# Performance work log

Hardware: AMD Instinct MI355X
Metric: run time of the kernel (lower is better)

Reference implementation:

```python
import jax, jax.numpy as jnp
import numpy as np
import math

B, C, K, H, W_SP = 16, 512, 64, 64, 64
STAGE_NUM = 2
THETA = 45


def _l2norm(x, axis):
    return x / (1e-6 + jnp.linalg.norm(x, axis=axis, keepdims=True))


def setup_inputs() -> dict:
    key = jax.random.key(0)
    k1, k2, k3, k4 = jax.random.split(key, 4)
    x = jax.random.normal(k1, (B, C, H, W_SP), dtype=jnp.float32)
    # conv1: 1x1 conv with bias, He init n = 1*1*C
    W1 = jax.random.normal(k2, (C, C), dtype=jnp.float32) * math.sqrt(2.0 / C)
    b1 = jnp.zeros((C,), dtype=jnp.float32)
    # conv2: 1x1 conv no bias + BN(gamma=1, beta=0)
    W2 = jax.random.normal(k3, (C, C), dtype=jnp.float32) * math.sqrt(2.0 / C)
    gamma = jnp.ones((C,), dtype=jnp.float32)
    beta = jnp.zeros((C,), dtype=jnp.float32)
    # mu buffer: normal(0, sqrt(2/k)), l2-normalized over channel dim
    mu0 = jax.random.normal(k4, (1, C, K), dtype=jnp.float32) * math.sqrt(2.0 / K)
    mu0 = _l2norm(mu0, axis=1)
    return {"x": x, "W1": W1, "b1": b1, "W2": W2, "gamma": gamma, "beta": beta, "mu0": mu0}


def reference(x, W1, b1, W2, gamma, beta, mu0):
    idn = x
    # conv1 (1x1)
    xc = jnp.einsum('bchw,oc->bohw', x, W1) + b1[None, :, None, None]
    b, c, h, w = xc.shape
    xf = xc.reshape(b, c, h * w)  # [b, c, n]
    mu = jnp.broadcast_to(mu0, (b, c, K))
    alpha0 = math.sin(math.radians(THETA)) ** 2
    beta0 = math.cos(math.radians(THETA)) ** 2
    v = K - 1
    # EM loop runs under torch.no_grad in the original -> stop_gradient
    xs = jax.lax.stop_gradient(xf)
    z = None
    for _ in range(STAGE_NUM):
        z = jnp.einsum('bcn,bck->bnk', xs, mu)  # [b, n, k]
        # V-E step: softmax / power-law blend
        z = alpha0 * jax.nn.softmax(z, axis=2) \
            + beta0 * (v + 1) / (v + 2.0 * jnp.linalg.norm(z, axis=2, keepdims=True))
        z_ = z / (1e-6 + z.sum(axis=1, keepdims=True))
        # V-M step
        mu = _l2norm(jnp.einsum('bcn,bnk->bck', xs, z_), axis=1)
    mu = jax.lax.stop_gradient(mu)
    z = jax.lax.stop_gradient(z)
    # reconstruction
    xr = jnp.einsum('bck,bnk->bcn', mu, z).reshape(b, c, h, w)
    xr = jax.nn.relu(xr)
    # conv2 (1x1, no bias) + BN (training-mode batch stats, eps=1e-5)
    y = jnp.einsum('bchw,oc->bohw', xr, W2)
    mean = y.mean(axis=(0, 2, 3))
    var = y.var(axis=(0, 2, 3))
    y = gamma[None, :, None, None] * (y - mean[None, :, None, None]) \
        * jax.lax.rsqrt(var + 1e-5)[None, :, None, None] + beta[None, :, None, None]
    out = jax.nn.relu(y + idn)
    return (out, mu, jnp.float32(THETA))
```

## Files before the change

### kernel.cpp

```cpp
#include <hip/hip_runtime.h>
#include <hip/hip_bf16.h>

#define B_ 16
#define C_ 512
#define K_ 64
#define N_ 4096
#define LDA 40

typedef unsigned short ushort_t;
typedef __attribute__((ext_vector_type(8))) short s16x8;
typedef __attribute__((ext_vector_type(4))) short s16x4;
typedef __attribute__((ext_vector_type(4))) float f32x4;

__device__ inline ushort_t f2bf(float f) {
    unsigned int u = __builtin_bit_cast(unsigned int, f);
    u = (u + 0x7FFFu + ((u >> 16) & 1u)) >> 16;
    return (ushort_t)u;
}
__device__ inline ushort_t f2bf_fast(float f) {
    unsigned int u = __builtin_bit_cast(unsigned int, f);
    return (ushort_t)((u + 0x8000u) >> 16);
}
__device__ inline float bf2f(ushort_t h) {
    unsigned int u = ((unsigned int)h) << 16;
    return __builtin_bit_cast(float, u);
}

template<int R>
__device__ inline void stage_tile(ushort_t* lds, const ushort_t* g, int gstride) {
    const int t = threadIdx.x;
    #pragma unroll
    for (int l = 0; l < R / 64; ++l) {
        int ch = t + l * 256;
        int row = ch >> 2, seg = ch & 3;
        s16x8 v = *(const s16x8*)(g + (size_t)row * gstride + seg * 8);
        *(s16x8*)(lds + row * LDA + seg * 8) = v;
    }
}

__global__ __launch_bounds__(256)
void cvtW_kernel(const float* __restrict__ W1, const float* __restrict__ W2,
                 ushort_t* __restrict__ W1b, ushort_t* __restrict__ W2b)
{
    int idx = blockIdx.x * 256 + threadIdx.x;
    const float* s; ushort_t* d; int off;
    if (idx < 32768) { s = W1; d = W1b; off = idx * 8; }
    else             { s = W2; d = W2b; off = (idx - 32768) * 8; }
    float4 a = *(const float4*)(s + off);
    float4 b = *(const float4*)(s + off + 4);
    s16x8 v;
    v[0] = (short)f2bf(a.x); v[1] = (short)f2bf(a.y);
    v[2] = (short)f2bf(a.z); v[3] = (short)f2bf(a.w);
    v[4] = (short)f2bf(b.x); v[5] = (short)f2bf(b.y);
    v[6] = (short)f2bf(b.z); v[7] = (short)f2bf(b.w);
    *(s16x8*)(d + off) = v;
}

__global__ __launch_bounds__(256)
void initmu_kernel(const float* __restrict__ mu0, ushort_t* __restrict__ mu_t)
{
    int idx = blockIdx.x * 256 + threadIdx.x;
    float v = mu0[idx];
    mu_t[(idx & 63) * C_ + (idx >> 6)] = f2bf(v);
}

__global__ __launch_bounds__(256)
void conv1_mfma(const ushort_t* __restrict__ W1b, const float* __restrict__ x,
                const float* __restrict__ b1, ushort_t* __restrict__ xf,
                ushort_t* __restrict__ xft)
{
    __shared__ ushort_t As[128 * LDA];
    __shared__ ushort_t Bs[128 * LDA];
    const int n0 = blockIdx.x * 128;
    const int o0 = blockIdx.y * 128;
    const int b  = blockIdx.z;
    const int t  = threadIdx.x;
    const int wid = t >> 6, lane = t & 63;
    const int wm = wid >> 1, wn = wid & 1;
    const int l15 = lane & 15, q = lane >> 4;

    const ushort_t* gA = W1b + (size_t)o0 * C_;
    const float*    xB = x + (size_t)b * C_ * N_ + n0;
    const int cg = t >> 5, ng = t & 31;

    f32x4 acc[4][4] = {};

    for (int c0 = 0; c0 < C_; c0 += 32) {
        __syncthreads();
        stage_tile<128>(As, gA + c0, C_);
        {
            const float* src = xB + (size_t)(c0 + cg * 4) * N_ + ng * 4;
            float4 f0 = *(const float4*)(src);
            float4 f1 = *(const float4*)(src + N_);
            float4 f2 = *(const float4*)(src + 2 * N_);
            float4 f3 = *(const float4*)(src + 3 * N_);
            ushort_t* dst = Bs + (ng * 4) * LDA + cg * 4;
            s16x4 v;
            v[0] = (short)f2bf_fast(f0.x); v[1] = (short)f2bf_fast(f1.x);
            v[2] = (short)f2bf_fast(f2.x); v[3] = (short)f2bf_fast(f3.x);
            *(s16x4*)(dst) = v;
            v[0] = (short)f2bf_fast(f0.y); v[1] = (short)f2bf_fast(f1.y);
            v[2] = (short)f2bf_fast(f2.y); v[3] = (short)f2bf_fast(f3.y);
            *(s16x4*)(dst + LDA) = v;
            v[0] = (short)f2bf_fast(f0.z); v[1] = (short)f2bf_fast(f1.z);
            v[2] = (short)f2bf_fast(f2.z); v[3] = (short)f2bf_fast(f3.z);
            *(s16x4*)(dst + 2 * LDA) = v;
            v[0] = (short)f2bf_fast(f0.w); v[1] = (short)f2bf_fast(f1.w);
            v[2] = (short)f2bf_fast(f2.w); v[3] = (short)f2bf_fast(f3.w);
            *(s16x4*)(dst + 3 * LDA) = v;
        }
        __syncthreads();
        s16x8 af[4], bf[4];
        #pragma unroll
        for (int m = 0; m < 4; ++m)
            af[m] = *(const s16x8*)&As[(wm * 64 + m * 16 + l15) * LDA + q * 8];
        #pragma unroll
        for (int n = 0; n < 4; ++n)
            bf[n] = *(const s16x8*)&Bs[(wn * 64 + n * 16 + l15) * LDA + q * 8];
        #pragma unroll
        for (int m = 0; m < 4; ++m)
            #pragma unroll
            for (int n = 0; n < 4; ++n)
                acc[m][n] = __builtin_amdgcn_mfma_f32_16x16x32_bf16(af[m], bf[n], acc[m][n], 0, 0, 0);
    }

    ushort_t* xfB  = xf  + (size_t)b * C_ * N_;
    ushort_t* xftB = xft + (size_t)b * N_ * C_;
    #pragma unroll
    for (int m = 0; m < 4; ++m) {
        int obase = o0 + wm * 64 + m * 16 + 4 * q;
        float bv[4];
        #pragma unroll
        for (int r = 0; r < 4; ++r) bv[r] = b1[obase + r];
        #pragma unroll
        for (int n = 0; n < 4; ++n) {
            int nn = n0 + wn * 64 + n * 16 + l15;
            s16x4 pk;
            #pragma unroll
            for (int r = 0; r < 4; ++r) {
                ushort_t h = f2bf(acc[m][n][r] + bv[r]);
                pk[r] = (short)h;
                xfB[(size_t)(obase + r) * N_ + nn] = h;
            }
            *(s16x4*)&xftB[(size_t)nn * C_ + obase] = pk;
        }
    }
}

__global__ __launch_bounds__(256)
void zfused_mfma(const ushort_t* __restrict__ mu_t, const ushort_t* __restrict__ xft,
                 ushort_t* __restrict__ zst, ushort_t* __restrict__ zs,
                 float* __restrict__ cs, int mustride)
{
    __shared__ char pool[64 * 133 * 4 + 64 * 132 * 2 + 128 * 2 * 4];
    float*    zt  = (float*)pool;
    ushort_t* zb  = (ushort_t*)(pool + 64 * 133 * 4);
    float*    csb = (float*)(pool + 64 * 133 * 4 + 64 * 132 * 2);
    ushort_t* As  = (ushort_t*)pool;
    ushort_t* Bs  = (ushort_t*)(pool + 64 * LDA * 2);

    const int n0 = blockIdx.x * 128;
    const int b  = blockIdx.y;
    const int t  = threadIdx.x;
    const int wid = t >> 6, lane = t & 63;
    const int wm = wid >> 1, wn = wid & 1;
    const int l15 = lane & 15, q = lane >> 4;

    const ushort_t* gA = mu_t + (size_t)b * mustride;
    const ushort_t* gB = xft + (size_t)b * N_ * C_ + (size_t)n0 * C_;

    f32x4 acc[2][4] = {};

    for (int c0 = 0; c0 < C_; c0 += 32) {
        __syncthreads();
        stage_tile<64>(As, gA + c0, C_);
        stage_tile<128>(Bs, gB + c0, C_);
        __syncthreads();
        s16x8 af[2], bf[4];
        #pragma unroll
        for (int m = 0; m < 2; ++m)
            af[m] = *(const s16x8*)&As[(wm * 32 + m * 16 + l15) * LDA + q * 8];
        #pragma unroll
        for (int n = 0; n < 4; ++n)
            bf[n] = *(const s16x8*)&Bs[(wn * 64 + n * 16 + l15) * LDA + q * 8];
        #pragma unroll
        for (int m = 0; m < 2; ++m)
            #pragma unroll
            for (int n = 0; n < 4; ++n)
                acc[m][n] = __builtin_amdgcn_mfma_f32_16x16x32_bf16(af[m], bf[n], acc[m][n], 0, 0, 0);
    }

    __syncthreads();
    #pragma unroll
    for (int m = 0; m < 2; ++m) {
        int kbase = wm * 32 + m * 16 + 4 * q;
        #pragma unroll
        for (int n = 0; n < 4; ++n) {
            int nl = wn * 64 + n * 16 + l15;
            #pragma unroll
            for (int r = 0; r < 4; ++r)
                zt[(kbase + r) * 133 + nl] = acc[m][n][r];
        }
    }
    __syncthreads();
    if (t < 128) {
        const float* col = zt + t;
        float mx = -1e30f, sq = 0.f;
        #pragma unroll
        for (int k = 0; k < K_; ++k) {
            float v = col[k * 133];
            mx = fmaxf(mx, v);
            sq += v * v;
        }
        float se = 0.f;
        #pragma unroll
        for (int k = 0; k < K_; ++k) {
            float e = __expf(col[k * 133] - mx);
            se += e;
            zb[k * 132 + t] = f2bf(e);
        }
        csb[t * 2]     = 0.5f / se;
        csb[t * 2 + 1] = 0.5f * 64.f / (63.f + 2.f * sqrtf(sq));
    }
    __syncthreads();
    ushort_t* zstB = zst + (size_t)b * K_ * N_;
    #pragma unroll
    for (int i = 0; i < 4; ++i) {
        int ch = t + 256 * i;
        int k = ch >> 4, seg = ch & 15;
        s16x8 e8 = *(const s16x8*)&zb[k * 132 + seg * 8];
        s16x8 o8;
        float sum = 0.f;
        #pragma unroll
        for (int j = 0; j < 8; ++j) {
            int nl = seg * 8 + j;
            float v = fmaf(bf2f((ushort_t)e8[j]), csb[nl * 2], csb[nl * 2 + 1]);
            sum += v;
            o8[j] = (short)f2bf(v);
        }
        *(s16x8*)&zstB[(size_t)k * N_ + n0 + seg * 8] = o8;
        #pragma unroll
        for (int off = 1; off < 16; off <<= 1) sum += __shfl_xor(sum, off);
        if ((t & 15) == 0) atomicAdd(&cs[b * K_ + k], sum);
    }
    ushort_t* zsB = zs + (size_t)b * N_ * K_;
    #pragma unroll
    for (int i = 0; i < 4; ++i) {
        int ch = t + 256 * i;
        int nl = ch >> 3, kseg = ch & 7;
        float sc = csb[nl * 2], bl = csb[nl * 2 + 1];
        s16x8 o8;
        #pragma unroll
        for (int j = 0; j < 8; ++j) {
            int j2 = (j + nl) & 7;
            float v = fmaf(bf2f(zb[(kseg * 8 + j2) * 132 + nl]), sc, bl);
            o8[j2] = (short)f2bf(v);
        }
        *(s16x8*)&zsB[(size_t)(n0 + nl) * K_ + kseg * 8] = o8;
    }
}

__global__ __launch_bounds__(256)
void mugemm_mfma(const ushort_t* __restrict__ zst, const ushort_t* __restrict__ xf,
                 const float* __restrict__ cs, float* __restrict__ macc)
{
    __shared__ ushort_t As[64 * LDA];
    __shared__ ushort_t Bs[128 * LDA];
    const int ns = blockIdx.x * 512;
    const int c0 = blockIdx.y * 128;
    const int b  = blockIdx.z;
    const int t  = threadIdx.x;
    const int wid = t >> 6, lane = t & 63;
    const int wm = wid >> 1, wn = wid & 1;
    const int l15 = lane & 15, q = lane >> 4;

    const ushort_t* gA = zst + (size_t)b * K_ * N_ + ns;
    const ushort_t* gB = xf + (size_t)b * C_ * N_ + (size_t)c0 * N_ + ns;

    f32x4 acc[2][4] = {};

    for (int nn0 = 0; nn0 < 512; nn0 += 32) {
        __syncthreads();
        stage_tile<64>(As, gA + nn0, N_);
        stage_tile<128>(Bs, gB + nn0, N_);
        __syncthreads();
        s16x8 af[2], bf[4];
        #pragma unroll
        for (int m = 0; m < 2; ++m)
            af[m] = *(const s16x8*)&As[(wm * 32 + m * 16 + l15) * LDA + q * 8];
        #pragma unroll
        for (int n = 0; n < 4; ++n)
            bf[n] = *(const s16x8*)&Bs[(wn * 64 + n * 16 + l15) * LDA + q * 8];
        #pragma unroll
        for (int m = 0; m < 2; ++m)
            #pragma unroll
            for (int n = 0; n < 4; ++n)
                acc[m][n] = __builtin_amdgcn_mfma_f32_16x16x32_bf16(af[m], bf[n], acc[m][n], 0, 0, 0);
    }

    float* mB = macc + (size_t)b * K_ * C_;
    #pragma unroll
    for (int m = 0; m < 2; ++m) {
        int kbase = wm * 32 + m * 16 + 4 * q;
        float ic[4];
        #pragma unroll
        for (int r = 0; r < 4; ++r) ic[r] = 1.f / (1e-6f + cs[b * K_ + kbase + r]);
        #pragma unroll
        for (int n = 0; n < 4; ++n) {
            int cc = c0 + wn * 64 + n * 16 + l15;
            #pragma unroll
            for (int r = 0; r < 4; ++r)
                atomicAdd(&mB[(size_t)(kbase + r) * C_ + cc], acc[m][n][r] * ic[r]);
        }
    }
}

__global__ __launch_bounds__(256)
void l2norm_t(const float* __restrict__ macc, ushort_t* __restrict__ mu_t,
              ushort_t* __restrict__ mu_b, float* __restrict__ mu_out,
              float* __restrict__ theta_out)
{
    int wid  = blockIdx.x * 4 + (threadIdx.x >> 6);
    int lane = threadIdx.x & 63;
    int b = wid >> 6, k = wid & 63;
    const float* src = macc + (size_t)b * K_ * C_ + (size_t)k * C_;
    float v[8], s = 0.f;
    #pragma unroll
    for (int i = 0; i < 8; ++i) { v[i] = src[lane + i * 64]; s += v[i] * v[i]; }
    #pragma unroll
    for (int off = 32; off > 0; off >>= 1) s += __shfl_xor(s, off);
    float inv = 1.f / (1e-6f + sqrtf(s));
    ushort_t* mt = mu_t + (size_t)b * K_ * C_ + (size_t)k * C_;
    ushort_t* mb = mu_b + (size_t)b * C_ * K_ + k;
    float*    mo = mu_out + (size_t)b * C_ * K_ + k;
    #pragma unroll
    for (int i = 0; i < 8; ++i) {
        int c = lane + i * 64;
        float val = v[i] * inv;
        mt[c] = f2bf(val);
        mb[(size_t)c * K_] = f2bf(val);
        mo[(size_t)c * K_] = val;
    }
    if (wid == 0 && lane == 0) *theta_out = 45.0f;
}

__global__ __launch_bounds__(256)
void recon_mfma(const ushort_t* __restrict__ mu_b, const ushort_t* __restrict__ zs,
                ushort_t* __restrict__ xrt)
{
    __shared__ ushort_t As[128 * LDA];
    __shared__ ushort_t Bs[128 * LDA];
    const int n0 = blockIdx.x * 128;
    const int c0 = blockIdx.y * 128;
    const int b  = blockIdx.z;
    const int t  = threadIdx.x;
    const int wid = t >> 6, lane = t & 63;
    const int wm = wid >> 1, wn = wid & 1;
    const int l15 = lane & 15, q = lane >> 4;

    const ushort_t* gA = mu_b + (size_t)b * C_ * K_ + (size_t)c0 * K_;
    const ushort_t* gB = zs + (size_t)b * N_ * K_ + (size_t)n0 * K_;

    f32x4 acc[4][4] = {};

    for (int k0 = 0; k0 < K_; k0 += 32) {
        __syncthreads();
        stage_tile<128>(As, gA + k0, K_);
        stage_tile<128>(Bs, gB + k0, K_);
        __syncthreads();
        s16x8 af[4], bf[4];
        #pragma unroll
        for (int m = 0; m < 4; ++m)
            af[m] = *(const s16x8*)&As[(wm * 64 + m * 16 + l15) * LDA + q * 8];
        #pragma unroll
        for (int n = 0; n < 4; ++n)
            bf[n] = *(const s16x8*)&Bs[(wn * 64 + n * 16 + l15) * LDA + q * 8];
        #pragma unroll
        for (int m = 0; m < 4; ++m)
            #pragma unroll
            for (int n = 0; n < 4; ++n)
                acc[m][n] = __builtin_amdgcn_mfma_f32_16x16x32_bf16(af[m], bf[n], acc[m][n], 0, 0, 0);
    }

    ushort_t* xB = xrt + (size_t)b * N_ * C_;
    #pragma unroll
    for (int m = 0; m < 4; ++m) {
        int cbase = c0 + wm * 64 + m * 16 + 4 * q;
        #pragma unroll
        for (int n = 0; n < 4; ++n) {
            int nn = n0 + wn * 64 + n * 16 + l15;
            s16x4 pk;
            #pragma unroll
            for (int r = 0; r < 4; ++r)
                pk[r] = (short)f2bf(fmaxf(acc[m][n][r], 0.f));
            *(s16x4*)&xB[(size_t)nn * C_ + cbase] = pk;
        }
    }
}

__global__ __launch_bounds__(256)
void conv2_mfma(const ushort_t* __restrict__ W2b, const ushort_t* __restrict__ xrt,
                float* __restrict__ y, float* __restrict__ ysum, float* __restrict__ ysq)
{
    __shared__ ushort_t As[128 * LDA];
    __shared__ ushort_t Bs[128 * LDA];
    __shared__ float sums[128][2];
    const int n0 = blockIdx.x * 128;
    const int o0 = blockIdx.y * 128;
    const int b  = blockIdx.z;
    const int t  = threadIdx.x;
    const int wid = t >> 6, lane = t & 63;
    const int wm = wid >> 1, wn = wid & 1;
    const int l15 = lane & 15, q = lane >> 4;

    const ushort_t* gA = W2b + (size_t)o0 * C_;
    const ushort_t* gB = xrt + (size_t)b * N_ * C_ + (size_t)n0 * C_;

    f32x4 acc[4][4] = {};

    for (int c0 = 0; c0 < C_; c0 += 32) {
        __syncthreads();
        stage_tile<128>(As, gA + c0, C_);
        stage_tile<128>(Bs, gB + c0, C_);
        __syncthreads();
        s16x8 af[4], bf[4];
        #pragma unroll
        for (int m = 0; m < 4; ++m)
            af[m] = *(const s16x8*)&As[(wm * 64 + m * 16 + l15) * LDA + q * 8];
        #pragma unroll
        for (int n = 0; n < 4; ++n)
            bf[n] = *(const s16x8*)&Bs[(wn * 64 + n * 16 + l15) * LDA + q * 8];
        #pragma unroll
        for (int m = 0; m < 4; ++m)
            #pragma unroll
            for (int n = 0; n < 4; ++n)
                acc[m][n] = __builtin_amdgcn_mfma_f32_16x16x32_bf16(af[m], bf[n], acc[m][n], 0, 0, 0);
    }

    float* yB = y + (size_t)b * C_ * N_;
    float ps[4][4], pq[4][4];
    #pragma unroll
    for (int m = 0; m < 4; ++m) {
        int obase = o0 + wm * 64 + m * 16 + 4 * q;
        #pragma unroll
        for (int r = 0; r < 4; ++r) { ps[m][r] = 0.f; pq[m][r] = 0.f; }
        #pragma unroll
        for (int n = 0; n < 4; ++n) {
            int nn = n0 + wn * 64 + n * 16 + l15;
            #pragma unroll
            for (int r = 0; r < 4; ++r) {
                float v = acc[m][n][r];
                yB[(size_t)(obase + r) * N_ + nn] = v;
                ps[m][r] += v;
                pq[m][r] = fmaf(v, v, pq[m][r]);
            }
        }
    }
    #pragma unroll
    for (int m = 0; m < 4; ++m)
        #pragma unroll
        for (int r = 0; r < 4; ++r)
            #pragma unroll
            for (int off = 1; off < 16; off <<= 1) {
                ps[m][r] += __shfl_xor(ps[m][r], off);
                pq[m][r] += __shfl_xor(pq[m][r], off);
            }
    __syncthreads();
    if (l15 == 0 && wn == 0) {
        #pragma unroll
        for (int m = 0; m < 4; ++m)
            #pragma unroll
            for (int r = 0; r < 4; ++r) {
                int ol = wm * 64 + m * 16 + 4 * q + r;
                sums[ol][0] = ps[m][r];
                sums[ol][1] = pq[m][r];
            }
    }
    __syncthreads();
    if (l15 == 0 && wn == 1) {
        #pragma unroll
        for (int m = 0; m < 4; ++m)
            #pragma unroll
            for (int r = 0; r < 4; ++r) {
                int ol = wm * 64 + m * 16 + 4 * q + r;
                sums[ol][0] += ps[m][r];
                sums[ol][1] += pq[m][r];
            }
    }
    __syncthreads();
    if (t < 128) {
        atomicAdd(&ysum[o0 + t], sums[t][0]);
        atomicAdd(&ysq[o0 + t],  sums[t][1]);
    }
}

__global__ __launch_bounds__(256)
void bnout_kernel(float* __restrict__ y, const float* __restrict__ x,
                  const float* __restrict__ gamma, const float* __restrict__ beta,
                  const float* __restrict__ ysum, const float* __restrict__ ysq)
{
    size_t i = (size_t)blockIdx.x * 256 + threadIdx.x;
    float4 vy = ((float4*)y)[i];
    float4 vx = ((const float4*)x)[i];
    int o = (int)((i >> 10) & (C_ - 1));
    const float inv_n = 1.f / (float)(B_ * N_);
    float mean = ysum[o] * inv_n;
    float var  = ysq[o] * inv_n - mean * mean;
    float istd = rsqrtf(var + 1e-5f);
    float sc = gamma[o] * istd;
    float sh = beta[o] - sc * mean;
    float4 r;
    r.x = fmaxf(fmaf(vy.x, sc, sh) + vx.x, 0.f);
    r.y = fmaxf(fmaf(vy.y, sc, sh) + vx.y, 0.f);
    r.z = fmaxf(fmaf(vy.z, sc, sh) + vx.z, 0.f);
    r.w = fmaxf(fmaf(vy.w, sc, sh) + vx.w, 0.f);
    ((float4*)y)[i] = r;
}

extern "C" void kernel_launch(void* const* d_in, const int* in_sizes, int n_in,
                              void* d_out, int out_size, void* d_ws, size_t ws_size,
                              hipStream_t stream)
{
    const float* x     = (const float*)d_in[0];
    const float* W1    = (const float*)d_in[1];
    const float* b1    = (const float*)d_in[2];
    const float* W2    = (const float*)d_in[3];
    const float* gamma = (const float*)d_in[4];
    const float* beta  = (const float*)d_in[5];
    const float* mu0   = (const float*)d_in[6];

    char* w = (char*)d_ws;
    ushort_t* xf   = (ushort_t*)w;  w += (size_t)B_ * C_ * N_ * 2;
    ushort_t* xft  = (ushort_t*)w;  w += (size_t)B_ * N_ * C_ * 2;
    ushort_t* W1b  = (ushort_t*)w;  w += (size_t)C_ * C_ * 2;
    ushort_t* W2b  = (ushort_t*)w;  w += (size_t)C_ * C_ * 2;
    ushort_t* mu_t = (ushort_t*)w;  w += (size_t)B_ * K_ * C_ * 2;
    ushort_t* mu_b = (ushort_t*)w;  w += (size_t)B_ * C_ * K_ * 2;
    float* cs      = (float*)w;     w += (size_t)B_ * K_ * 4;
    float* macc    = (float*)w;     w += (size_t)B_ * K_ * C_ * 4;
    float* ysum    = (float*)w;     w += C_ * 4;
    float* ysq     = (float*)w;     w += C_ * 4;

    ushort_t* xrt = xf;

    float* y         = (float*)d_out;
    float* mu_out    = (float*)d_out + (size_t)B_ * C_ * N_;
    float* theta_out = mu_out + (size_t)B_ * C_ * K_;
    ushort_t* zst = (ushort_t*)(y + (size_t)8  * 1024 * 1024);
    ushort_t* zs  = (ushort_t*)(y + (size_t)16 * 1024 * 1024);

    cvtW_kernel<<<256, 256, 0, stream>>>(W1, W2, W1b, W2b);
    initmu_kernel<<<128, 256, 0, stream>>>(mu0, mu_t);
    hipMemsetAsync(ysum, 0, 2 * C_ * 4, stream);

    conv1_mfma<<<dim3(32, 4, 16), 256, 0, stream>>>(W1b, x, b1, xf, xft);

    for (int s = 0; s < 2; ++s) {
        hipMemsetAsync(cs, 0, (size_t)B_ * K_ * 4 + (size_t)B_ * K_ * C_ * 4, stream);
        zfused_mfma<<<dim3(32, 16), 256, 0, stream>>>(mu_t, xft, zst, zs, cs,
                                                      s == 0 ? 0 : K_ * C_);
        mugemm_mfma<<<dim3(8, 4, 16), 256, 0, stream>>>(zst, xf, cs, macc);
        l2norm_t<<<256, 256, 0, stream>>>(macc, mu_t, mu_b, mu_out, theta_out);
    }

    recon_mfma<<<dim3(32, 4, 16), 256, 0, stream>>>(mu_b, zs, xrt);
    conv2_mfma<<<dim3(32, 4, 16), 256, 0, stream>>>(W2b, xrt, y, ysum, ysq);
    bnout_kernel<<<dim3(B_ * C_ * N_ / 4 / 256), 256, 0, stream>>>(y, x, gamma, beta, ysum, ysq);
}
```

Baseline: 573.4 us.

## Stage conv GEMM tiles via direct global-to-LDS loads with XOR-swizzled layouts

Adds a separate kernel that converts x to transposed bf16 with an XOR-swizzled channel layout. conv1 and conv2 now stage tiles with global_load_lds 16-byte transfers into unpadded LDS instead of register round trips. W1/W2 conversion and recon output are written in the same swizzled order so LDS fragment reads avoid bank conflicts without padding. This adds an extra pass over x and reuses the output buffer as scratch, in exchange for cheaper GEMM staging.

```diff
diff --git a/kernel.cpp b/kernel.cpp
--- a/kernel.cpp
+++ b/kernel.cpp
@@ -24,6 +24,12 @@
 __device__ inline float bf2f(ushort_t h) {
     unsigned int u = ((unsigned int)h) << 16;
     return __builtin_bit_cast(float, u);
+}
+
+__device__ inline void gload16(const ushort_t* g, ushort_t* l) {
+    __builtin_amdgcn_global_load_lds(
+        (const __attribute__((address_space(1))) void*)g,
+        (__attribute__((address_space(3))) void*)l, 16, 0, 0);
 }
 
 template<int R>
@@ -53,7 +59,9 @@
     v[2] = (short)f2bf(a.z); v[3] = (short)f2bf(a.w);
     v[4] = (short)f2bf(b.x); v[5] = (short)f2bf(b.y);
     v[6] = (short)f2bf(b.z); v[7] = (short)f2bf(b.w);
-    *(s16x8*)(d + off) = v;
+    int o = off >> 9, c = off & 511;
+    int dst = o * C_ + (c & ~31) + 8 * (((c >> 3) & 3) ^ ((o >> 1) & 3));
+    *(s16x8*)(d + dst) = v;
 }
 
 __global__ __launch_bounds__(256)
@@ -65,12 +73,52 @@
 }
 
 __global__ __launch_bounds__(256)
-void conv1_mfma(const ushort_t* __restrict__ W1b, const float* __restrict__ x,
+void xcvt_kernel(const float* __restrict__ x, ushort_t* __restrict__ xbt)
+{
+    __shared__ __align__(16) ushort_t lds[64 * 72];
+    const int n0 = blockIdx.x * 64;
+    const int c0 = blockIdx.y * 64;
+    const int b  = blockIdx.z;
+    const int t  = threadIdx.x;
+    const int cq = t >> 4, nq = t & 15;
+    const float* src = x + ((size_t)b * C_ + c0 + cq * 4) * N_ + n0 + nq * 4;
+    float4 f0 = *(const float4*)(src);
+    float4 f1 = *(const float4*)(src + N_);
+    float4 f2 = *(const float4*)(src + 2 * N_);
+    float4 f3 = *(const float4*)(src + 3 * N_);
+    ushort_t* ld = lds + (nq * 4) * 72 + cq * 4;
+    s16x4 v;
+    v[0] = (short)f2bf_fast(f0.x); v[1] = (short)f2bf_fast(f1.x);
+    v[2] = (short)f2bf_fast(f2.x); v[3] = (short)f2bf_fast(f3.x);
+    *(s16x4*)(ld) = v;
+    v[0] = (short)f2bf_fast(f0.y); v[1] = (short)f2bf_fast(f1.y);
+    v[2] = (short)f2bf_fast(f2.y); v[3] = (short)f2bf_fast(f3.y);
+    *(s16x4*)(ld + 72) = v;
+    v[0] = (short)f2bf_fast(f0.z); v[1] = (short)f2bf_fast(f1.z);
+    v[2] = (short)f2bf_fast(f2.z); v[3] = (short)f2bf_fast(f3.z);
+    *(s16x4*)(ld + 144) = v;
+    v[0] = (short)f2bf_fast(f0.w); v[1] = (short)f2bf_fast(f1.w);
+    v[2] = (short)f2bf_fast(f2.w); v[3] = (short)f2bf_fast(f3.w);
+    *(s16x4*)(ld + 216) = v;
+    __syncthreads();
+    ushort_t* dst = xbt + ((size_t)b * N_ + n0) * C_ + c0;
+    #pragma unroll
+    for (int i = 0; i < 2; ++i) {
+        int ch = t + 256 * i;
+        int row = ch >> 3, seg = ch & 7;
+        s16x8 w = *(const s16x8*)&lds[row * 72 + seg * 8];
+        int cc = (seg >> 2) * 32 + 8 * ((seg & 3) ^ ((row >> 1) & 3));
+        *(s16x8*)(dst + (size_t)row * C_ + cc) = w;
+    }
+}
+
+__global__ __launch_bounds__(256)
+void conv1_mfma(const ushort_t* __restrict__ W1b, const ushort_t* __restrict__ xbt,
                 const float* __restrict__ b1, ushort_t* __restrict__ xf,
                 ushort_t* __restrict__ xft)
 {
-    __shared__ ushort_t As[128 * LDA];
-    __shared__ ushort_t Bs[128 * LDA];
+    __shared__ __align__(16) ushort_t As[128 * 32];
+    __shared__ __align__(16) ushort_t Bs[128 * 32];
     const int n0 = blockIdx.x * 128;
     const int o0 = blockIdx.y * 128;
     const int b  = blockIdx.z;
@@ -78,45 +126,33 @@
     const int wid = t >> 6, lane = t & 63;
     const int wm = wid >> 1, wn = wid & 1;
     const int l15 = lane & 15, q = lane >> 4;
+    const int gsw = (q ^ ((l15 >> 1) & 3)) * 8;
 
     const ushort_t* gA = W1b + (size_t)o0 * C_;
-    const float*    xB = x + (size_t)b * C_ * N_ + n0;
-    const int cg = t >> 5, ng = t & 31;
+    const ushort_t* gB = xbt + ((size_t)b * N_ + n0) * C_;
+    const size_t choff  = (size_t)(t >> 2) * C_ + (t & 3) * 8;
+    const size_t choff2 = choff + (size_t)64 * C_;
+
+    int aoff[4], boff[4];
+    #pragma unroll
+    for (int m = 0; m < 4; ++m) aoff[m] = (wm * 64 + m * 16 + l15) * 32 + gsw;
+    #pragma unroll
+    for (int n = 0; n < 4; ++n) boff[n] = (wn * 64 + n * 16 + l15) * 32 + gsw;
 
     f32x4 acc[4][4] = {};
 
     for (int c0 = 0; c0 < C_; c0 += 32) {
         __syncthreads();
-        stage_tile<128>(As, gA + c0, C_);
-        {
-            const float* src = xB + (size_t)(c0 + cg * 4) * N_ + ng * 4;
-            float4 f0 = *(const float4*)(src);
-            float4 f1 = *(const float4*)(src + N_);
-            float4 f2 = *(const float4*)(src + 2 * N_);
-            float4 f3 = *(const float4*)(src + 3 * N_);
-            ushort_t* dst = Bs + (ng * 4) * LDA + cg * 4;
-            s16x4 v;
-            v[0] = (short)f2bf_fast(f0.x); v[1] = (short)f2bf_fast(f1.x);
-            v[2] = (short)f2bf_fast(f2.x); v[3] = (short)f2bf_fast(f3.x);
-            *(s16x4*)(dst) = v;
-            v[0] = (short)f2bf_fast(f0.y); v[1] = (short)f2bf_fast(f1.y);
-            v[2] = (short)f2bf_fast(f2.y); v[3] = (short)f2bf_fast(f3.y);
-            *(s16x4*)(dst + LDA) = v;
-            v[0] = (short)f2bf_fast(f0.z); v[1] = (short)f2bf_fast(f1.z);
-            v[2] = (short)f2bf_fast(f2.z); v[3] = (short)f2bf_fast(f3.z);
-            *(s16x4*)(dst + 2 * LDA) = v;
-            v[0] = (short)f2bf_fast(f0.w); v[1] = (short)f2bf_fast(f1.w);
-            v[2] = (short)f2bf_fast(f2.w); v[3] = (short)f2bf_fast(f3.w);
-            *(s16x4*)(dst + 3 * LDA) = v;
-        }
+        gload16(gA + choff  + c0, &As[t * 8]);
+        gload16(gA + choff2 + c0, &As[t * 8 + 2048]);
+        gload16(gB + choff  + c0, &Bs[t * 8]);
+        gload16(gB + choff2 + c0, &Bs[t * 8 + 2048]);
         __syncthreads();
         s16x8 af[4], bf[4];
         #pragma unroll
-        for (int m = 0; m < 4; ++m)
-            af[m] = *(const s16x8*)&As[(wm * 64 + m * 16 + l15) * LDA + q * 8];
-        #pragma unroll
-        for (int n = 0; n < 4; ++n)
-            bf[n] = *(const s16x8*)&Bs[(wn * 64 + n * 16 + l15) * LDA + q * 8];
+        for (int m = 0; m < 4; ++m) af[m] = *(const s16x8*)&As[aoff[m]];
+        #pragma unroll
+        for (int n = 0; n < 4; ++n) bf[n] = *(const s16x8*)&Bs[boff[n]];
         #pragma unroll
         for (int m = 0; m < 4; ++m)
             #pragma unroll
@@ -152,7 +188,7 @@
                  ushort_t* __restrict__ zst, ushort_t* __restrict__ zs,
                  float* __restrict__ cs, int mustride)
 {
-    __shared__ char pool[64 * 133 * 4 + 64 * 132 * 2 + 128 * 2 * 4];
+    __shared__ __align__(16) char pool[64 * 133 * 4 + 64 * 132 * 2 + 128 * 2 * 4];
     float*    zt  = (float*)pool;
     ushort_t* zb  = (ushort_t*)(pool + 64 * 133 * 4);
     float*    csb = (float*)(pool + 64 * 133 * 4 + 64 * 132 * 2);
@@ -264,8 +300,8 @@
 void mugemm_mfma(const ushort_t* __restrict__ zst, const ushort_t* __restrict__ xf,
                  const float* __restrict__ cs, float* __restrict__ macc)
 {
-    __shared__ ushort_t As[64 * LDA];
-    __shared__ ushort_t Bs[128 * LDA];
+    __shared__ __align__(16) ushort_t As[64 * LDA];
+    __shared__ __align__(16) ushort_t Bs[128 * LDA];
     const int ns = blockIdx.x * 512;
     const int c0 = blockIdx.y * 128;
     const int b  = blockIdx.z;
@@ -348,8 +384,8 @@
 void recon_mfma(const ushort_t* __restrict__ mu_b, const ushort_t* __restrict__ zs,
                 ushort_t* __restrict__ xrt)
 {
-    __shared__ ushort_t As[128 * LDA];
-    __shared__ ushort_t Bs[128 * LDA];
+    __shared__ __align__(16) ushort_t As[128 * LDA];
+    __shared__ __align__(16) ushort_t Bs[128 * LDA];
     const int n0 = blockIdx.x * 128;
     const int c0 = blockIdx.y * 128;
     const int b  = blockIdx.z;
@@ -383,9 +419,11 @@
     }
 
     ushort_t* xB = xrt + (size_t)b * N_ * C_;
+    const int swn = (l15 >> 1) & 3;
     #pragma unroll
     for (int m = 0; m < 4; ++m) {
         int cbase = c0 + wm * 64 + m * 16 + 4 * q;
+        int cswz  = (cbase & ~31) + 8 * (((cbase >> 3) & 3) ^ swn) + (cbase & 7);
         #pragma unroll
         for (int n = 0; n < 4; ++n) {
             int nn = n0 + wn * 64 + n * 16 + l15;
@@ -393,7 +431,7 @@
             #pragma unroll
             for (int r = 0; r < 4; ++r)
                 pk[r] = (short)f2bf(fmaxf(acc[m][n][r], 0.f));
-            *(s16x4*)&xB[(size_t)nn * C_ + cbase] = pk;
+            *(s16x4*)&xB[(size_t)nn * C_ + cswz] = pk;
         }
     }
 }
@@ -402,8 +440,8 @@
 void conv2_mfma(const ushort_t* __restrict__ W2b, const ushort_t* __restrict__ xrt,
                 float* __restrict__ y, float* __restrict__ ysum, float* __restrict__ ysq)
 {
-    __shared__ ushort_t As[128 * LDA];
-    __shared__ ushort_t Bs[128 * LDA];
+    __shared__ __align__(16) ushort_t As[128 * 32];
+    __shared__ __align__(16) ushort_t Bs[128 * 32];
     __shared__ float sums[128][2];
     const int n0 = blockIdx.x * 128;
     const int o0 = blockIdx.y * 128;
@@ -412,24 +450,33 @@
     const int wid = t >> 6, lane = t & 63;
     const int wm = wid >> 1, wn = wid & 1;
     const int l15 = lane & 15, q = lane >> 4;
+    const int gsw = (q ^ ((l15 >> 1) & 3)) * 8;
 
     const ushort_t* gA = W2b + (size_t)o0 * C_;
-    const ushort_t* gB = xrt + (size_t)b * N_ * C_ + (size_t)n0 * C_;
+    const ushort_t* gB = xrt + ((size_t)b * N_ + n0) * C_;
+    const size_t choff  = (size_t)(t >> 2) * C_ + (t & 3) * 8;
+    const size_t choff2 = choff + (size_t)64 * C_;
+
+    int aoff[4], boff[4];
+    #pragma unroll
+    for (int m = 0; m < 4; ++m) aoff[m] = (wm * 64 + m * 16 + l15) * 32 + gsw;
+    #pragma unroll
+    for (int n = 0; n < 4; ++n) boff[n] = (wn * 64 + n * 16 + l15) * 32 + gsw;
 
     f32x4 acc[4][4] = {};
 
     for (int c0 = 0; c0 < C_; c0 += 32) {
         __syncthreads();
-        stage_tile<128>(As, gA + c0, C_);
-        stage_tile<128>(Bs, gB + c0, C_);
+        gload16(gA + choff  + c0, &As[t * 8]);
+        gload16(gA + choff2 + c0, &As[t * 8 + 2048]);
+        gload16(gB + choff  + c0, &Bs[t * 8]);
+        gload16(gB + choff2 + c0, &Bs[t * 8 + 2048]);
         __syncthreads();
         s16x8 af[4], bf[4];
         #pragma unroll
-        for (int m = 0; m < 4; ++m)
-            af[m] = *(const s16x8*)&As[(wm * 64 + m * 16 + l15) * LDA + q * 8];
-        #pragma unroll
-        for (int n = 0; n < 4; ++n)
-            bf[n] = *(const s16x8*)&Bs[(wn * 64 + n * 16 + l15) * LDA + q * 8];
+        for (int m = 0; m < 4; ++m) af[m] = *(const s16x8*)&As[aoff[m]];
+        #pragma unroll
+        for (int n = 0; n < 4; ++n) bf[n] = *(const s16x8*)&Bs[boff[n]];
         #pragma unroll
         for (int m = 0; m < 4; ++m)
             #pragma unroll
@@ -546,14 +593,16 @@
     float* y         = (float*)d_out;
     float* mu_out    = (float*)d_out + (size_t)B_ * C_ * N_;
     float* theta_out = mu_out + (size_t)B_ * C_ * K_;
-    ushort_t* zst = (ushort_t*)(y + (size_t)8  * 1024 * 1024);
-    ushort_t* zs  = (ushort_t*)(y + (size_t)16 * 1024 * 1024);
+    ushort_t* xbt = (ushort_t*)d_out;
+    ushort_t* zst = (ushort_t*)((char*)d_out + (size_t)80 * 1024 * 1024);
+    ushort_t* zs  = (ushort_t*)((char*)d_out + (size_t)96 * 1024 * 1024);
 
     cvtW_kernel<<<256, 256, 0, stream>>>(W1, W2, W1b, W2b);
     initmu_kernel<<<128, 256, 0, stream>>>(mu0, mu_t);
     hipMemsetAsync(ysum, 0, 2 * C_ * 4, stream);
 
-    conv1_mfma<<<dim3(32, 4, 16), 256, 0, stream>>>(W1b, x, b1, xf, xft);
+    xcvt_kernel<<<dim3(64, 8, 16), 256, 0, stream>>>(x, xbt);
+    conv1_mfma<<<dim3(32, 4, 16), 256, 0, stream>>>(W1b, xbt, b1, xf, xft);
 
     for (int s = 0; s < 2; ++s) {
         hipMemsetAsync(cs, 0, (size_t)B_ * K_ * 4 + (size_t)B_ * K_ * C_ * 4, stream);
```

After: 580.5 us. About the same (+1.2%).
